# Kernel optimization log

Hardware: AMD Instinct MI355X
Metric: run time of the kernel (lower is better)

Reference implementation:

```python
import jax, jax.numpy as jnp
import numpy as np

B, S, E, H, FF = 4, 2048, 1024, 16, 4096
DK = E // H
EPS = 1e-5


def setup_inputs() -> dict:
    key = jax.random.key(0)
    ks = jax.random.split(key, 16)
    sc = 0.02
    return {
        "x": jax.random.normal(ks[0], (B, S, E), jnp.float32),
        "Wq": jax.random.normal(ks[1], (E, E), jnp.float32) * sc,
        "Wk": jax.random.normal(ks[2], (E, E), jnp.float32) * sc,
        "Wv": jax.random.normal(ks[3], (E, E), jnp.float32) * sc,
        "Wo": jax.random.normal(ks[4], (E, E), jnp.float32) * sc,
        "theta": jax.random.normal(ks[5], (DK,), jnp.float32),
        "Wcq": jax.random.normal(ks[6], (E, E), jnp.float32) * sc,
        "ln1_g": jnp.ones((E,), jnp.float32),
        "ln1_b": jnp.zeros((E,), jnp.float32),
        "W1": jax.random.normal(ks[7], (E, FF), jnp.float32) * sc,
        "b1": jnp.zeros((FF,), jnp.float32),
        "W2": jax.random.normal(ks[8], (FF, E), jnp.float32) * sc,
        "b2": jnp.zeros((E,), jnp.float32),
        "ln2_g": jnp.ones((E,), jnp.float32),
        "ln2_b": jnp.zeros((E,), jnp.float32),
    }


def _layernorm(x, g, b):
    mu = jnp.mean(x, axis=-1, keepdims=True)
    var = jnp.mean(jnp.square(x - mu), axis=-1, keepdims=True)
    return (x - mu) * jax.lax.rsqrt(var + EPS) * g + b


def reference(x, Wq, Wk, Wv, Wo, theta, Wcq, ln1_g, ln1_b, W1, b1, W2, b2, ln2_g, ln2_b):
    mix = 0.5
    # classical multi-head attention
    def heads(t):  # [B,S,E] -> [B,H,S,DK]
        return t.reshape(B, S, H, DK).transpose(0, 2, 1, 3)
    q = heads(x @ Wq)
    k = heads(x @ Wk)
    v = heads(x @ Wv)
    scores = jnp.einsum("bhqd,bhkd->bhqk", q, k) / jnp.sqrt(jnp.float32(DK))
    attn = jax.nn.softmax(scores, axis=-1)
    ctx = jnp.einsum("bhqk,bhkd->bhqd", attn, v)
    ctx = ctx.transpose(0, 2, 1, 3).reshape(B, S, E)
    classical = ctx @ Wo
    # quantum heads: RX(x)RX(theta)|0>, <Z> = cos(x + theta), same theta shared per head
    qh = jnp.cos(x.reshape(B, S, H, DK) + theta)  # broadcast over wires
    quantum = qh.reshape(B, S, E) @ Wcq
    attn_out = mix * classical + (1.0 - mix) * quantum
    x1 = _layernorm(x + attn_out, ln1_g, ln1_b)
    ffn = jax.nn.relu(x1 @ W1 + b1) @ W2 + b2
    return _layernorm(x1 + ffn, ln2_g, ln2_b)
```

## Files before the change

### kernel.cpp

```cpp
#include <hip/hip_runtime.h>
#include <hip/hip_bf16.h>

typedef __bf16 bf16_t;
typedef bf16_t bf16x8 __attribute__((ext_vector_type(8)));
typedef bf16_t bf16x4v __attribute__((ext_vector_type(4)));
typedef float f32x4 __attribute__((ext_vector_type(4)));

static constexpr int EE = 1024;
static constexpr int SS = 2048;
static constexpr int DK = 64;
static constexpr float QSCALE = 0.125f * 1.44269504f;

__device__ __forceinline__ void gload_lds16(const void* g, void* l) {
  __builtin_amdgcn_global_load_lds(
      (__attribute__((address_space(1))) void*)g,
      (__attribute__((address_space(3))) void*)l, 16, 0, 0);
}

__device__ __forceinline__ f32x4 mfma16(bf16x8 a, bf16x8 b, f32x4 c) {
  return __builtin_amdgcn_mfma_f32_16x16x32_bf16(a, b, c, 0, 0, 0);
}

template<int OFF>
__device__ __forceinline__ bf16x4v tr8(unsigned va) {
  bf16x4v d;
  asm volatile("ds_read_b64_tr_b16 %0, %1 offset:%c2"
               : "=v"(d) : "v"(va), "i"(OFF));
  return d;
}

__global__ void __launch_bounds__(256) prep_x_kernel(
    const float* __restrict__ x, const float* __restrict__ theta,
    bf16_t* __restrict__ xbf, bf16_t* __restrict__ A2)
{
  const long t = (long)blockIdx.x * 256 + threadIdx.x;
  const long e0 = t * 8;
  const int col = (int)(e0 & (EE - 1));
  const long row = e0 >> 10;
  const float4 v0 = *(const float4*)&x[e0];
  const float4 v1 = *(const float4*)&x[e0 + 4];
  float xs[8] = {v0.x, v0.y, v0.z, v0.w, v1.x, v1.y, v1.z, v1.w};
  const int d0 = col & (DK - 1);
  bf16x8 xb, qb;
#pragma unroll
  for (int j = 0; j < 8; ++j) {
    xb[j] = (bf16_t)xs[j];
    qb[j] = (bf16_t)__cosf(xs[j] + theta[d0 + j]);
  }
  *(bf16x8*)&xbf[e0] = xb;
  *(bf16x8*)&A2[row * 2048 + EE + col] = qb;
}

__global__ void __launch_bounds__(256) transpose_w_kernel(
    const float* __restrict__ src, bf16_t* __restrict__ dst,
    int N, long dstride, long dcol0)
{
  __shared__ float tile[32][33];
  const int tx = threadIdx.x, ty = threadIdx.y;
  const long n0 = (long)blockIdx.x * 32, k0 = (long)blockIdx.y * 32;
#pragma unroll
  for (int j = 0; j < 4; ++j)
    tile[ty + j * 8][tx] = src[(k0 + ty + j * 8) * N + n0 + tx];
  __syncthreads();
#pragma unroll
  for (int j = 0; j < 4; ++j)
    dst[(n0 + ty + j * 8) * dstride + dcol0 + k0 + tx] = (bf16_t)tile[tx][ty + j * 8];
}

template<int MODE, int TN>
__global__ void __launch_bounds__(512, 2) gemm256(
    const bf16_t* __restrict__ A, const bf16_t* __restrict__ Bt,
    void* __restrict__ C, int M, int N, int K,
    const float* __restrict__ aux1, const bf16_t* __restrict__ aux2)
{
  constexpr int MB  = (TN == 256) ? 8 : 4;
  constexpr int MBH = MB / 2;
  constexpr int NB  = 4;
  __shared__ bf16_t As[4][256 * 32];
  __shared__ bf16_t Bs[4][TN * 32];
  const int tid = threadIdx.x;
  const int lane = tid & 63, wid = tid >> 6;
  const int wr = (TN == 256) ? (wid >> 2) : (wid >> 1);
  const int wc = (TN == 256) ? (wid & 3) : (wid & 1);
  const int lr = lane & 15, lk = lane >> 4;
  const int gx = gridDim.x;
  const int nwg = gx * gridDim.y;
  const int bid = blockIdx.y * gx + blockIdx.x;
  const int swz = (bid & 7) * (nwg >> 3) + (bid >> 3);
  const long m0 = (long)(swz / gx) * 256;
  const long n0 = (long)(swz % gx) * TN;

  const int rql = lane >> 2;
  const int sl  = lane & 3;
  const int rA0 = wid * 32 + rql, rA1 = wid * 32 + 16 + rql;
  const bf16_t* sA0 = &A [(m0 + rA0) * K + 8 * (sl ^ ((rA0 >> 1) & 3))];
  const bf16_t* sA1 = &A [(m0 + rA1) * K + 8 * (sl ^ ((rA1 >> 1) & 3))];
  const int rB0 = (TN == 256) ? (wid * 32 + rql) : (wid * 16 + rql);
  const int rB1 = wid * 32 + 16 + rql;
  const bf16_t* sB0 = &Bt[(n0 + rB0) * K + 8 * (sl ^ ((rB0 >> 1) & 3))];
  const bf16_t* sB1 = &Bt[(n0 + rB1) * K + 8 * (sl ^ ((rB1 >> 1) & 3))];
  const int loA = wid * 1024;
  const int loB = (TN == 256) ? wid * 1024 : wid * 512;

  f32x4 acc[MB][NB] = {};
  const int NKT = K / 32;

  auto stA = [&](int t) {
    const int s = t & 3;
    gload_lds16(sA0 + (long)t * 32, &As[s][loA]);
    gload_lds16(sA1 + (long)t * 32, &As[s][loA + 512]);
  };
  auto stB = [&](int t) {
    const int s = t & 3;
    gload_lds16(sB0 + (long)t * 32, &Bs[s][loB]);
    if constexpr (TN == 256)
      gload_lds16(sB1 + (long)t * 32, &Bs[s][loB + 512]);
  };

  stA(0); stB(0); stA(1); stB(1); stA(2); stB(2);
  if constexpr (TN == 256) { asm volatile("s_waitcnt vmcnt(8)" ::: "memory"); }
  else                     { asm volatile("s_waitcnt vmcnt(6)" ::: "memory"); }
  __builtin_amdgcn_s_barrier();

  for (int t = 0; t < NKT; ++t) {
    const int s = t & 3;
    bf16x8 bfr[NB], af1[MBH], af2[MBH];
#pragma unroll
    for (int nb = 0; nb < NB; ++nb) {
      const int rw = wc * 64 + nb * 16 + lr;
      bfr[nb] = *(const bf16x8*)&Bs[s][rw * 32 + (lk ^ ((rw >> 1) & 3)) * 8];
    }
#pragma unroll
    for (int mb = 0; mb < MBH; ++mb) {
      const int rw = wr * (MB * 16) + mb * 16 + lr;
      af1[mb] = *(const bf16x8*)&As[s][rw * 32 + (lk ^ ((rw >> 1) & 3)) * 8];
    }
    __builtin_amdgcn_sched_barrier(0);
#pragma unroll
    for (int mb = 0; mb < MBH; ++mb) {
      const int rw = wr * (MB * 16) + (MBH + mb) * 16 + lr;
      af2[mb] = *(const bf16x8*)&As[s][rw * 32 + (lk ^ ((rw >> 1) & 3)) * 8];
    }
    if (t + 3 < NKT) { stA(t + 3); stB(t + 3); }
    if constexpr (MBH == 4) { asm volatile("s_waitcnt lgkmcnt(4)" ::: "memory"); }
    else                    { asm volatile("s_waitcnt lgkmcnt(2)" ::: "memory"); }
    __builtin_amdgcn_sched_barrier(0);
    __builtin_amdgcn_s_setprio(1);
#pragma unroll
    for (int mb = 0; mb < MBH; ++mb)
#pragma unroll
      for (int nb = 0; nb < NB; ++nb)
        acc[mb][nb] = mfma16(af1[mb], bfr[nb], acc[mb][nb]);
    __builtin_amdgcn_s_setprio(0);
    asm volatile("s_waitcnt lgkmcnt(0)" ::: "memory");
    __builtin_amdgcn_sched_barrier(0);
    __builtin_amdgcn_s_setprio(1);
#pragma unroll
    for (int mb = 0; mb < MBH; ++mb)
#pragma unroll
      for (int nb = 0; nb < NB; ++nb)
        acc[MBH + mb][nb] = mfma16(af2[mb], bfr[nb], acc[MBH + mb][nb]);
    __builtin_amdgcn_s_setprio(0);
    if (t + 3 < NKT) {
      if constexpr (TN == 256) { asm volatile("s_waitcnt vmcnt(8)" ::: "memory"); }
      else                     { asm volatile("s_waitcnt vmcnt(6)" ::: "memory"); }
    } else if (t + 3 == NKT) {
      if constexpr (TN == 256) { asm volatile("s_waitcnt vmcnt(4)" ::: "memory"); }
      else                     { asm volatile("s_waitcnt vmcnt(3)" ::: "memory"); }
    } else if (t + 2 == NKT) {
      asm volatile("s_waitcnt vmcnt(0)" ::: "memory");
    }
    __builtin_amdgcn_s_barrier();
  }

#pragma unroll
  for (int mb = 0; mb < MB; ++mb)
#pragma unroll
    for (int nb = 0; nb < NB; ++nb)
#pragma unroll
      for (int i = 0; i < 4; ++i) {
        const long r = m0 + wr * (MB * 16) + mb * 16 + lk * 4 + i;
        const long cc = n0 + wc * 64 + nb * 16 + lr;
        float v = acc[mb][nb][i];
        if constexpr (MODE == 0) {
          if (cc < 1024) v *= QSCALE;
          ((bf16_t*)C)[r * N + cc] = (bf16_t)v;
        } else if constexpr (MODE == 1) {
          ((float*)C)[r * N + cc] = 0.5f * v + aux1[r * N + cc];
        } else if constexpr (MODE == 2) {
          ((bf16_t*)C)[r * N + cc] = (bf16_t)fmaxf(v + aux1[cc], 0.0f);
        } else {
          ((float*)C)[r * N + cc] = v + aux1[cc] + (float)aux2[r * N + cc];
        }
      }
}

__global__ void __launch_bounds__(256, 2) attn_kernel(
    const bf16_t* __restrict__ QKV, bf16_t* __restrict__ Ctx)
{
  __shared__ bf16_t Ks[2][64 * 72];
  __shared__ bf16_t Vt[2][64 * 64];
  const int tid = threadIdx.x;
  const int lane = tid & 63, w = tid >> 6;
  const int lr = lane & 15, lk = lane >> 4;
  const int bh = blockIdx.x, b = bh >> 4, h = bh & 15;
  const long rowbase = (long)b * SS;
  const int q0 = blockIdx.y * 128;
  const int qcol = h * 64, kcol = EE + h * 64, vcol = 2 * EE + h * 64;
  constexpr int NT = SS / 64;

  bf16x8 qf[2][2];
#pragma unroll
  for (int mb = 0; mb < 2; ++mb)
#pragma unroll
    for (int ks = 0; ks < 2; ++ks)
      qf[mb][ks] = *(const bf16x8*)&QKV[
          (rowbase + q0 + w * 32 + mb * 16 + lr) * 3072 + qcol + ks * 32 + lk * 8];

  const int sr = tid >> 3;
  const int g  = tid & 7;
  const int d0 = g * 8;

  const unsigned vtr_base =
      (unsigned)(uintptr_t)(__attribute__((address_space(3))) void*)&Vt[0][0]
      + 2u * (unsigned)(lr + lk * 64);

  bf16x8 kreg[2], vreg[2];
  auto load_kv = [&](int t) {
#pragma unroll
    for (int it = 0; it < 2; ++it) {
      const long r = rowbase + (long)t * 64 + sr + it * 32;
      kreg[it] = *(const bf16x8*)&QKV[r * 3072 + kcol + d0];
      vreg[it] = *(const bf16x8*)&QKV[r * 3072 + vcol + d0];
    }
  };
  auto write_kv = [&](int buf) {
#pragma unroll
    for (int it = 0; it < 2; ++it) {
      const int r = sr + it * 32;
      *(bf16x8*)&Ks[buf][r * 72 + d0] = kreg[it];
      const int va = (d0 >> 4) * 1024 + (r >> 2) * 64 + (r & 3) * 16 + (d0 & 15);
      *(bf16x8*)&Vt[buf][va] = vreg[it];
    }
  };

  f32x4 oacc[2][4] = {};
  float lsum[2] = {0.0f, 0.0f};

  load_kv(0);
  write_kv(0);

  for (int t = 0; t < NT; ++t) {
    const int buf = t & 1;
    __syncthreads();
    if (t + 1 < NT) load_kv(t + 1);

    bf16x8 kf[4][2];
#pragma unroll
    for (int nb = 0; nb < 4; ++nb)
#pragma unroll
      for (int ks = 0; ks < 2; ++ks)
        kf[nb][ks] = *(const bf16x8*)&Ks[buf][(nb * 16 + lr) * 72 + ks * 32 + lk * 8];

    f32x4 sacc[2][4] = {};
    __builtin_amdgcn_s_setprio(1);
#pragma unroll
    for (int mb = 0; mb < 2; ++mb)
#pragma unroll
      for (int nb = 0; nb < 4; ++nb)
#pragma unroll
        for (int ks = 0; ks < 2; ++ks)
          sacc[mb][nb] = mfma16(kf[nb][ks], qf[mb][ks], sacc[mb][nb]);
    __builtin_amdgcn_s_setprio(0);

    const unsigned va = vtr_base + (unsigned)buf * 8192u;
    bf16x4v vlo[4][2], vhi[4][2];
    vlo[0][0] = tr8<   0>(va);  vhi[0][0] = tr8< 512>(va);
    vlo[0][1] = tr8<1024>(va);  vhi[0][1] = tr8<1536>(va);
    vlo[1][0] = tr8<2048>(va);  vhi[1][0] = tr8<2560>(va);
    vlo[1][1] = tr8<3072>(va);  vhi[1][1] = tr8<3584>(va);
    vlo[2][0] = tr8<4096>(va);  vhi[2][0] = tr8<4608>(va);
    vlo[2][1] = tr8<5120>(va);  vhi[2][1] = tr8<5632>(va);
    vlo[3][0] = tr8<6144>(va);  vhi[3][0] = tr8<6656>(va);
    vlo[3][1] = tr8<7168>(va);  vhi[3][1] = tr8<7680>(va);

#pragma unroll
    for (int mb = 0; mb < 2; ++mb) {
      float psum = 0.0f;
      bf16x8 pf[2];
#pragma unroll
      for (int nb = 0; nb < 4; ++nb)
#pragma unroll
        for (int i = 0; i < 4; ++i) {
          const float pv = exp2f(sacc[mb][nb][i]);
          psum += pv;
          pf[nb >> 1][(nb & 1) * 4 + i] = (bf16_t)pv;
        }
      lsum[mb] += psum;
      asm volatile("s_waitcnt lgkmcnt(0)" ::: "memory");
      __builtin_amdgcn_sched_barrier(0);
      __builtin_amdgcn_s_setprio(1);
#pragma unroll
      for (int nb = 0; nb < 4; ++nb)
#pragma unroll
        for (int ks = 0; ks < 2; ++ks) {
          const bf16x8 vf = __builtin_shufflevector(
              vlo[nb][ks], vhi[nb][ks], 0, 1, 2, 3, 4, 5, 6, 7);
          oacc[mb][nb] = mfma16(pf[ks], vf, oacc[mb][nb]);
        }
      __builtin_amdgcn_s_setprio(0);
    }

    if (t + 1 < NT) write_kv((t + 1) & 1);
  }

#pragma unroll
  for (int mb = 0; mb < 2; ++mb) {
    float l = lsum[mb];
    l += __shfl_xor(l, 16);
    l += __shfl_xor(l, 32);
    float li[4];
#pragma unroll
    for (int i = 0; i < 4; ++i) li[i] = 1.0f / __shfl(l, lk * 4 + i);
#pragma unroll
    for (int nb = 0; nb < 4; ++nb)
#pragma unroll
      for (int i = 0; i < 4; ++i) {
        const long r = rowbase + q0 + w * 32 + mb * 16 + lk * 4 + i;
        Ctx[r * 2048 + h * 64 + nb * 16 + lr] = (bf16_t)(oacc[mb][nb][i] * li[i]);
      }
  }
}

__device__ __forceinline__ void ln_reduce(const float4& v, int tid,
                                          float& mu, float& rs) {
  float s = v.x + v.y + v.z + v.w;
  float ss = v.x * v.x + v.y * v.y + v.z * v.z + v.w * v.w;
#pragma unroll
  for (int off = 1; off < 64; off <<= 1) {
    s += __shfl_xor(s, off);
    ss += __shfl_xor(ss, off);
  }
  __shared__ float wsum[4], wsq[4];
  if ((tid & 63) == 0) { wsum[tid >> 6] = s; wsq[tid >> 6] = ss; }
  __syncthreads();
  s = wsum[0] + wsum[1] + wsum[2] + wsum[3];
  ss = wsq[0] + wsq[1] + wsq[2] + wsq[3];
  mu = s * (1.0f / EE);
  rs = rsqrtf(ss * (1.0f / EE) - mu * mu + 1e-5f);
}

__global__ void __launch_bounds__(256) ln_bf16_kernel(
    const float* __restrict__ pre, const float* __restrict__ g,
    const float* __restrict__ bt, bf16_t* __restrict__ out)
{
  const int r = blockIdx.x, tid = threadIdx.x;
  const long base = (long)r * EE + tid * 4;
  const float4 v = *(const float4*)&pre[base];
  float mu, rs;
  ln_reduce(v, tid, mu, rs);
  const float4 gv = *(const float4*)&g[tid * 4];
  const float4 bv = *(const float4*)&bt[tid * 4];
  bf16x4v o;
  o[0] = (bf16_t)((v.x - mu) * rs * gv.x + bv.x);
  o[1] = (bf16_t)((v.y - mu) * rs * gv.y + bv.y);
  o[2] = (bf16_t)((v.z - mu) * rs * gv.z + bv.z);
  o[3] = (bf16_t)((v.w - mu) * rs * gv.w + bv.w);
  *(bf16x4v*)&out[base] = o;
}

__global__ void __launch_bounds__(256) ln_f32_kernel(
    const float* __restrict__ pre, const float* __restrict__ g,
    const float* __restrict__ bt, float* __restrict__ out)
{
  const int r = blockIdx.x, tid = threadIdx.x;
  const long base = (long)r * EE + tid * 4;
  const float4 v = *(const float4*)&pre[base];
  float mu, rs;
  ln_reduce(v, tid, mu, rs);
  const float4 gv = *(const float4*)&g[tid * 4];
  const float4 bv = *(const float4*)&bt[tid * 4];
  float4 o;
  o.x = (v.x - mu) * rs * gv.x + bv.x;
  o.y = (v.y - mu) * rs * gv.y + bv.y;
  o.z = (v.z - mu) * rs * gv.z + bv.z;
  o.w = (v.w - mu) * rs * gv.w + bv.w;
  *(float4*)&out[base] = o;
}

extern "C" void kernel_launch(void* const* d_in, const int* in_sizes, int n_in,
                              void* d_out, int out_size, void* d_ws, size_t ws_size,
                              hipStream_t stream)
{
  (void)in_sizes; (void)n_in; (void)out_size; (void)ws_size;
  const float* x     = (const float*)d_in[0];
  const float* Wq    = (const float*)d_in[1];
  const float* Wk    = (const float*)d_in[2];
  const float* Wv    = (const float*)d_in[3];
  const float* Wo    = (const float*)d_in[4];
  const float* theta = (const float*)d_in[5];
  const float* Wcq   = (const float*)d_in[6];
  const float* ln1g  = (const float*)d_in[7];
  const float* ln1b  = (const float*)d_in[8];
  const float* W1    = (const float*)d_in[9];
  const float* b1    = (const float*)d_in[10];
  const float* W2    = (const float*)d_in[11];
  const float* b2    = (const float*)d_in[12];
  const float* ln2g  = (const float*)d_in[13];
  const float* ln2b  = (const float*)d_in[14];

  char* ws = (char*)d_ws;
  const size_t MB = 1ull << 20;
  bf16_t* xbf    = (bf16_t*)(ws + 0);
  bf16_t* QKV    = (bf16_t*)(ws + 16 * MB);
  float*  preLN1 = (float*)(ws + 16 * MB);
  bf16_t* A2     = (bf16_t*)(ws + 64 * MB);
  float*  preLN2 = (float*)(ws + 64 * MB);
  bf16_t* H1     = (bf16_t*)(ws + 96 * MB);
  bf16_t* BtQKV  = (bf16_t*)(ws + 160 * MB);
  bf16_t* Bt2    = (bf16_t*)(ws + 166 * MB);
  bf16_t* BtW1   = (bf16_t*)(ws + 170 * MB);
  bf16_t* BtW2   = (bf16_t*)(ws + 178 * MB);

  dim3 tb(32, 8);
  prep_x_kernel<<<4096, 256, 0, stream>>>(x, theta, xbf, A2);
  transpose_w_kernel<<<dim3(32, 32), tb, 0, stream>>>(Wq,  BtQKV,              1024, 1024, 0);
  transpose_w_kernel<<<dim3(32, 32), tb, 0, stream>>>(Wk,  BtQKV + 1024*1024,  1024, 1024, 0);
  transpose_w_kernel<<<dim3(32, 32), tb, 0, stream>>>(Wv,  BtQKV + 2048*1024,  1024, 1024, 0);
  transpose_w_kernel<<<dim3(32, 32), tb, 0, stream>>>(Wo,  Bt2,  1024, 2048, 0);
  transpose_w_kernel<<<dim3(32, 32), tb, 0, stream>>>(Wcq, Bt2,  1024, 2048, 1024);
  transpose_w_kernel<<<dim3(128, 32), tb, 0, stream>>>(W1, BtW1, 4096, 1024, 0);
  transpose_w_kernel<<<dim3(32, 128), tb, 0, stream>>>(W2, BtW2, 1024, 4096, 0);

  gemm256<0, 128><<<dim3(24, 32), 512, 0, stream>>>(xbf, BtQKV, QKV, 8192, 3072, 1024, nullptr, nullptr);
  attn_kernel<<<dim3(64, 16), 256, 0, stream>>>(QKV, A2);
  gemm256<1, 128><<<dim3(8, 32), 512, 0, stream>>>(A2, Bt2, preLN1, 8192, 1024, 2048, x, nullptr);
  ln_bf16_kernel<<<8192, 256, 0, stream>>>(preLN1, ln1g, ln1b, xbf);
  gemm256<2, 256><<<dim3(16, 32), 512, 0, stream>>>(xbf, BtW1, H1, 8192, 4096, 1024, b1, nullptr);
  gemm256<3, 128><<<dim3(8, 32), 512, 0, stream>>>(H1, BtW2, preLN2, 8192, 1024, 4096, b2, xbf);
  ln_f32_kernel<<<8192, 256, 0, stream>>>(preLN2, ln2g, ln2b, (float*)d_out);
}
```

Measured before the change: 452.9 us.

## Stage attention K/V tiles via direct global-to-LDS loads and merge weight transposes

The attention kernel now moves K and V tiles straight from global memory into LDS with global_load_lds. K uses an XOR-swizzled layout in place of the padded layout, and V is loaded with an address mapping that reproduces the transposed-read layout. This removes the register staging and the separate LDS write step, and frees registers. Separately, the seven weight transpose launches are merged into one kernel that picks its segment by block index, cutting launch overhead. The async LDS loads depend on the existing barrier and waitcnt placement being correct for the double buffer.

After: 440.3 us. 2.8% less time.

```diff
diff --git a/kernel.cpp b/kernel.cpp
--- a/kernel.cpp
+++ b/kernel.cpp
@@ -51,13 +51,36 @@
   *(bf16x8*)&A2[row * 2048 + EE + col] = qb;
 }
 
-__global__ void __launch_bounds__(256) transpose_w_kernel(
-    const float* __restrict__ src, bf16_t* __restrict__ dst,
-    int N, long dstride, long dcol0)
-{
+__global__ void __launch_bounds__(256) transpose_all_kernel(
+    const float* __restrict__ Wq, const float* __restrict__ Wk,
+    const float* __restrict__ Wv, const float* __restrict__ Wo,
+    const float* __restrict__ Wcq, const float* __restrict__ W1,
+    const float* __restrict__ W2,
+    bf16_t* __restrict__ BtQKV, bf16_t* __restrict__ Bt2,
+    bf16_t* __restrict__ BtW1, bf16_t* __restrict__ BtW2)
+{
+  const int bid = blockIdx.x;
+  const float* src; bf16_t* dst; int N; long dstride, dcol0; int bx, by;
+  if (bid < 5120) {
+    const int seg = bid >> 10, r = bid & 1023;
+    bx = r & 31; by = r >> 5; N = 1024;
+    if      (seg == 0) { src = Wq;  dst = BtQKV;               dstride = 1024; dcol0 = 0; }
+    else if (seg == 1) { src = Wk;  dst = BtQKV + 1024 * 1024; dstride = 1024; dcol0 = 0; }
+    else if (seg == 2) { src = Wv;  dst = BtQKV + 2048 * 1024; dstride = 1024; dcol0 = 0; }
+    else if (seg == 3) { src = Wo;  dst = Bt2;                 dstride = 2048; dcol0 = 0; }
+    else               { src = Wcq; dst = Bt2;                 dstride = 2048; dcol0 = 1024; }
+  } else if (bid < 9216) {
+    const int r = bid - 5120;
+    src = W1; dst = BtW1; N = 4096; dstride = 1024; dcol0 = 0;
+    bx = r & 127; by = r >> 7;
+  } else {
+    const int r = bid - 9216;
+    src = W2; dst = BtW2; N = 1024; dstride = 4096; dcol0 = 0;
+    bx = r & 31; by = r >> 5;
+  }
   __shared__ float tile[32][33];
   const int tx = threadIdx.x, ty = threadIdx.y;
-  const long n0 = (long)blockIdx.x * 32, k0 = (long)blockIdx.y * 32;
+  const long n0 = (long)bx * 32, k0 = (long)by * 32;
 #pragma unroll
   for (int j = 0; j < 4; ++j)
     tile[ty + j * 8][tx] = src[(k0 + ty + j * 8) * N + n0 + tx];
@@ -198,7 +221,7 @@
 __global__ void __launch_bounds__(256, 2) attn_kernel(
     const bf16_t* __restrict__ QKV, bf16_t* __restrict__ Ctx)
 {
-  __shared__ bf16_t Ks[2][64 * 72];
+  __shared__ bf16_t Ks[2][64 * 64];
   __shared__ bf16_t Vt[2][64 * 64];
   const int tid = threadIdx.x;
   const int lane = tid & 63, w = tid >> 6;
@@ -217,50 +240,44 @@
       qf[mb][ks] = *(const bf16x8*)&QKV[
           (rowbase + q0 + w * 32 + mb * 16 + lr) * 3072 + qcol + ks * 32 + lk * 8];
 
-  const int sr = tid >> 3;
-  const int g  = tid & 7;
-  const int d0 = g * 8;
+  const int ksl = ((lane & 7) ^ ((lane >> 3) & 7)) * 8;
+  const bf16_t* sK0 = &QKV[(rowbase + (2 * w + 0) * 8 + (lane >> 3)) * 3072 + kcol + ksl];
+  const bf16_t* sK1 = &QKV[(rowbase + (2 * w + 1) * 8 + (lane >> 3)) * 3072 + kcol + ksl];
+  const int vk = 4 * (lane >> 3) + ((lane >> 1) & 3);
+  const int vd = 16 * w + 8 * (lane & 1);
+  const bf16_t* sV0 = &QKV[(rowbase + vk) * 3072 + vcol + vd];
+  const bf16_t* sV1 = &QKV[(rowbase + 32 + vk) * 3072 + vcol + vd];
+
+  auto stage = [&](int t) {
+    const int buf = t & 1;
+    const long off = (long)t * 64 * 3072;
+    gload_lds16(sK0 + off, &Ks[buf][(2 * w + 0) * 512]);
+    gload_lds16(sK1 + off, &Ks[buf][(2 * w + 1) * 512]);
+    gload_lds16(sV0 + off, &Vt[buf][(2 * w + 0) * 512]);
+    gload_lds16(sV1 + off, &Vt[buf][(2 * w + 1) * 512]);
+  };
 
   const unsigned vtr_base =
       (unsigned)(uintptr_t)(__attribute__((address_space(3))) void*)&Vt[0][0]
       + 2u * (unsigned)(lr + lk * 64);
 
-  bf16x8 kreg[2], vreg[2];
-  auto load_kv = [&](int t) {
-#pragma unroll
-    for (int it = 0; it < 2; ++it) {
-      const long r = rowbase + (long)t * 64 + sr + it * 32;
-      kreg[it] = *(const bf16x8*)&QKV[r * 3072 + kcol + d0];
-      vreg[it] = *(const bf16x8*)&QKV[r * 3072 + vcol + d0];
-    }
-  };
-  auto write_kv = [&](int buf) {
-#pragma unroll
-    for (int it = 0; it < 2; ++it) {
-      const int r = sr + it * 32;
-      *(bf16x8*)&Ks[buf][r * 72 + d0] = kreg[it];
-      const int va = (d0 >> 4) * 1024 + (r >> 2) * 64 + (r & 3) * 16 + (d0 & 15);
-      *(bf16x8*)&Vt[buf][va] = vreg[it];
-    }
-  };
-
   f32x4 oacc[2][4] = {};
   float lsum[2] = {0.0f, 0.0f};
 
-  load_kv(0);
-  write_kv(0);
+  stage(0);
 
   for (int t = 0; t < NT; ++t) {
     const int buf = t & 1;
     __syncthreads();
-    if (t + 1 < NT) load_kv(t + 1);
+    if (t + 1 < NT) stage(t + 1);
 
     bf16x8 kf[4][2];
 #pragma unroll
     for (int nb = 0; nb < 4; ++nb)
 #pragma unroll
       for (int ks = 0; ks < 2; ++ks)
-        kf[nb][ks] = *(const bf16x8*)&Ks[buf][(nb * 16 + lr) * 72 + ks * 32 + lk * 8];
+        kf[nb][ks] = *(const bf16x8*)&Ks[buf][
+            (nb * 16 + lr) * 64 + ((ks * 4 + lk) ^ (lr & 7)) * 8];
 
     f32x4 sacc[2][4] = {};
     __builtin_amdgcn_s_setprio(1);
@@ -310,8 +327,6 @@
         }
       __builtin_amdgcn_s_setprio(0);
     }
-
-    if (t + 1 < NT) write_kv((t + 1) & 1);
   }
 
 #pragma unroll
@@ -422,15 +437,9 @@
   bf16_t* BtW1   = (bf16_t*)(ws + 170 * MB);
   bf16_t* BtW2   = (bf16_t*)(ws + 178 * MB);
 
-  dim3 tb(32, 8);
   prep_x_kernel<<<4096, 256, 0, stream>>>(x, theta, xbf, A2);
-  transpose_w_kernel<<<dim3(32, 32), tb, 0, stream>>>(Wq,  BtQKV,              1024, 1024, 0);
-  transpose_w_kernel<<<dim3(32, 32), tb, 0, stream>>>(Wk,  BtQKV + 1024*1024,  1024, 1024, 0);
-  transpose_w_kernel<<<dim3(32, 32), tb, 0, stream>>>(Wv,  BtQKV + 2048*1024,  1024, 1024, 0);
-  transpose_w_kernel<<<dim3(32, 32), tb, 0, stream>>>(Wo,  Bt2,  1024, 2048, 0);
-  transpose_w_kernel<<<dim3(32, 32), tb, 0, stream>>>(Wcq, Bt2,  1024, 2048, 1024);
-  transpose_w_kernel<<<dim3(128, 32), tb, 0, stream>>>(W1, BtW1, 4096, 1024, 0);
-  transpose_w_kernel<<<dim3(32, 128), tb, 0, stream>>>(W2, BtW2, 1024, 4096, 0);
+  transpose_all_kernel<<<13312, dim3(32, 8), 0, stream>>>(
+      Wq, Wk, Wv, Wo, Wcq, W1, W2, BtQKV, Bt2, BtW1, BtW2);
 
   gemm256<0, 128><<<dim3(24, 32), 512, 0, stream>>>(xbf, BtQKV, QKV, 8192, 3072, 1024, nullptr, nullptr);
   attn_kernel<<<dim3(64, 16), 256, 0, stream>>>(QKV, A2);
```
